# Performance work log

Hardware: AMD Instinct MI355X
Metric: run time of the kernel (lower is better)

## Reference

```python
import jax, jax.numpy as jnp
import numpy as np

B = 1024   # batch
N = 512    # points per sample (fixed by Linear(512,128))
G = 32     # voxel grid side (fixed: 5 stride-2 convs must reach 1^3)
CH = [1, 4, 16, 32, 64, 128]
BN_EPS = 1e-5


def _basis():
    # PointEmbed sinusoidal basis: hidden_dim=48 -> 8 freqs per axis, [3, 24]
    e = (2.0 ** np.arange(8)).astype(np.float32) * np.pi
    z = np.zeros(8, np.float32)
    b = np.stack([np.concatenate([e, z, z]),
                  np.concatenate([z, e, z]),
                  np.concatenate([z, z, e])])
    return jnp.asarray(b)


def setup_inputs() -> dict:
    key = jax.random.key(0)
    ks = jax.random.split(key, 16)
    inp = {
        "voxels": jax.random.normal(ks[0], (B, 1, G, G, G), jnp.float32),
        "centers": jax.random.uniform(ks[1], (B, N, 3), jnp.float32) * 2.0 - 1.0,
    }
    for i in range(5):
        cin, cout = CH[i], CH[i + 1]
        inp[f"W{i+1}"] = jax.random.normal(ks[2 + i], (cout, cin, 3, 3, 3), jnp.float32) * 0.05
        inp[f"b{i+1}"] = jnp.zeros((cout,), jnp.float32)
        inp[f"g{i+1}"] = jnp.ones((cout,), jnp.float32)
        inp[f"beta{i+1}"] = jnp.zeros((cout,), jnp.float32)
    inp["pe_w"] = jax.random.normal(ks[7], (51, 128), jnp.float32) * 0.05  # Linear(48+3, 128)
    inp["pe_b"] = jnp.zeros((128,), jnp.float32)
    inp["f1_w"] = jax.random.normal(ks[8], (128, 1), jnp.float32) * 0.05   # ff_128_1
    inp["f1_b"] = jnp.zeros((1,), jnp.float32)
    inp["f2_w"] = jax.random.normal(ks[9], (512, 128), jnp.float32) * 0.05  # ff_512_128
    inp["f2_b"] = jnp.zeros((128,), jnp.float32)
    return inp


def _conv_bn_relu(x, W, b, g, beta):
    # SparseConv3d(k=3, s=2, p=1) on fully-occupied grid == dense conv; BN in batch-stats mode
    y = jax.lax.conv_general_dilated(
        x, W, window_strides=(2, 2, 2), padding=[(1, 1)] * 3,
        dimension_numbers=("NCDHW", "OIDHW", "NCDHW"))
    y = y + b[None, :, None, None, None]
    m = jnp.mean(y, axis=(0, 2, 3, 4), keepdims=True)
    v = jnp.var(y, axis=(0, 2, 3, 4), keepdims=True)
    y = (y - m) * jax.lax.rsqrt(v + BN_EPS)
    y = y * g[None, :, None, None, None] + beta[None, :, None, None, None]
    return jax.nn.relu(y)


def reference(voxels, centers,
              W1, b1, g1, beta1, W2, b2, g2, beta2, W3, b3, g3, beta3,
              W4, b4, g4, beta4, W5, b5, g5, beta5,
              pe_w, pe_b, f1_w, f1_b, f2_w, f2_b):
    # --- PointEmbed branch ---
    basis = _basis()                                      # [3, 24]
    proj = jnp.einsum("bnd,de->bne", centers, basis)      # [B, N, 24]
    emb = jnp.concatenate([jnp.sin(proj), jnp.cos(proj), centers], axis=2)  # [B, N, 51]
    xc = emb @ pe_w + pe_b                                # [B, N, 128]
    xc = (xc @ f1_w + f1_b)[..., 0]                       # [B, N=512]
    xc = xc @ f2_w + f2_b                                 # [B, 128]
    # --- sparse conv stack (dense-occupancy equivalent) ---
    x = voxels
    for W, b, g, be in ((W1, b1, g1, beta1), (W2, b2, g2, beta2),
                        (W3, b3, g3, beta3), (W4, b4, g4, beta4),
                        (W5, b5, g5, beta5)):
        x = _conv_bn_relu(x, W, b, g, be)
    x = x.reshape(-1, 128)                                # [B,128,1,1,1] -> [B,128]
    return x + xc
```

## Files before the change

### kernel.cpp

```cpp
#include <hip/hip_runtime.h>
#include <hip/hip_bf16.h>

#ifndef M_PI
#define M_PI 3.14159265358979323846
#endif

#define BN_EPS 1e-5f

#define OFF_Y1   0ull
#define OFF_Y2   16777216ull
#define OFF_Y3   25165824ull
#define OFF_Y4   27262976ull
#define OFF_Y5   27787264ull
#define OFF_S    27918336ull
#define OFF_W2G  28442624ull
#define OFF_W3G  28444352ull
#define OFF_W5G  28458176ull
#define OFF_U    28523712ull
#define OFF_SP1  28523776ull
#define OFF_SP2  28524288ull
#define OFF_SP3  28526336ull
#define OFF_SP4  28530432ull
#define OFF_SP5  28538624ull
#define SP_TOTAL 31232
#define OFF_W4G  OFF_Y1

__device__ __forceinline__ float wred(float v) {
    for (int m = 32; m; m >>= 1) v += __shfl_xor(v, m, 64);
    return v;
}

__device__ __forceinline__ void async_copy16(const void* g, void* l) {
    __builtin_amdgcn_global_load_lds((const __attribute__((address_space(1))) void*)g,
                                     (__attribute__((address_space(3))) void*)l,
                                     16, 0, 0);
}

__device__ __forceinline__ unsigned short f2bf(float f) {
    unsigned int x = __float_as_uint(f);
    unsigned int r = (x + 0x7fffu + ((x >> 16) & 1u)) >> 16;
    return (unsigned short)r;
}
__device__ __forceinline__ float bf2f(unsigned short u) {
    return __uint_as_float(((unsigned int)u) << 16);
}

__global__ void k_prep_w(const float* __restrict__ W2, const float* __restrict__ W3,
                         const float* __restrict__ W5,
                         float* __restrict__ w2g, float* __restrict__ w3g,
                         float* __restrict__ w5g, float* __restrict__ sp) {
    int idx = blockIdx.x * 256 + threadIdx.x;
    if (idx < 1728) {
        int co = idx & 15; int r = idx >> 4; int tap = r % 27; int ci = r / 27;
        w2g[idx] = W2[(co * 4 + ci) * 27 + tap];
        return;
    }
    idx -= 1728;
    if (idx < 13824) {
        int co = idx & 31; int r = idx >> 5; int tap = r % 27; int ci = r / 27;
        w3g[idx] = W3[(co * 16 + ci) * 27 + tap];
        return;
    }
    idx -= 13824;
    if (idx < 65536) {
        int co = idx & 127; int k = idx >> 7;
        int dx = k & 1, dy = (k >> 1) & 1, dz = (k >> 2) & 1, ci = k >> 3;
        w5g[idx] = W5[(co * 64 + ci) * 27 + (dz + 1) * 9 + (dy + 1) * 3 + (dx + 1)];
        return;
    }
    idx -= 65536;
    if (idx < SP_TOTAL) sp[idx] = 0.f;
}

__global__ void k_prep_w4(const float* __restrict__ W4, float* __restrict__ w4g) {
    int idx = blockIdx.x * 256 + threadIdx.x;
    if (idx < 55296) {
        int co = idx & 63; int r = idx >> 6;
        int tap = r % 27, ci = r / 27;
        w4g[idx] = W4[(co * 32 + ci) * 27 + tap];
    }
}

__global__ void k_prep_u(const float* __restrict__ pe_w, const float* __restrict__ pe_b,
                         const float* __restrict__ f1_w, const float* __restrict__ f1_b,
                         float* __restrict__ u) {
    int t = threadIdx.x;
    if (t < 51) {
        float acc = 0.f;
        for (int j = 0; j < 128; j++) acc += pe_w[t * 128 + j] * f1_w[j];
        u[t] = acc;
    } else if (t == 51) {
        float acc = f1_b[0];
        for (int j = 0; j < 128; j++) acc += pe_b[j] * f1_w[j];
        u[51] = acc;
    }
}

__global__ __launch_bounds__(256) void k_pe(const float* __restrict__ centers,
                                            const float* __restrict__ u,
                                            float* __restrict__ s) {
    __shared__ float us[52];
    int t = threadIdx.x;
    if (t < 52) us[t] = u[t];
    __syncthreads();
    int idx = blockIdx.x * 256 + t;
    float c3[3];
    c3[0] = centers[idx * 3 + 0];
    c3[1] = centers[idx * 3 + 1];
    c3[2] = centers[idx * 3 + 2];
    float acc = us[51] + c3[0] * us[48] + c3[1] * us[49] + c3[2] * us[50];
#pragma unroll
    for (int a = 0; a < 3; a++) {
#pragma unroll
        for (int f = 0; f < 8; f++) {
            float ang = c3[a] * (float)(M_PI * (double)(1 << f));
            float sv, cv;
            sincosf(ang, &sv, &cv);
            acc += sv * us[a * 8 + f] + cv * us[24 + a * 8 + f];
        }
    }
    s[idx] = acc;
}

__global__ __launch_bounds__(256) void k_c1(const float* __restrict__ vox,
                                            const float* __restrict__ W1,
                                            const float* __restrict__ b1,
                                            unsigned short* __restrict__ y1b,
                                            float* __restrict__ sp1) {
    __shared__ __align__(16) float slab[9 * 1024];
    __shared__ __align__(16) float wl[112];
    __shared__ float red2[32];
    int bid = blockIdx.x;
    int b = bid >> 1, q = bid & 1;
    int t = threadIdx.x;
    const float* vb = vox + (size_t)b * 32768;
    int wu = __builtin_amdgcn_readfirstlane(t >> 6);

    if (t < 108) { int tap = t >> 2, co = t & 3; wl[t] = W1[co * 27 + tap]; }
    if (q == 0) ((float4*)slab)[t] = make_float4(0.f, 0.f, 0.f, 0.f);

    int p0 = 16 * q;
    int s0 = q ? 7 : 0;
    {
        int s = s0;
        for (int i = 0; i < 5; i++) {
            int p = p0 - 1 + i;
            if (p >= 0) async_copy16(vb + p * 1024 + t * 4, slab + s * 1024 + wu * 256);
            s++; if (s == 9) s = 0;
        }
    }
    int yo = t >> 4, xo = t & 15;
    int e = 2 * xo;
    int eA = (e >= 2) ? e - 2 : 0;
    float mx0 = xo ? 1.f : 0.f;
    int iyc[3]; float myv[3];
#pragma unroll
    for (int ky = 0; ky < 3; ky++) {
        int iy = 2 * yo + ky - 1;
        myv[ky] = (iy < 0) ? 0.f : 1.f;
        iyc[ky] = (iy < 0) ? 0 : iy;
    }
    float bb0 = b1[0], bb1 = b1[1], bb2 = b1[2], bb3 = b1[3];
    float sums[4] = {0.f, 0.f, 0.f, 0.f}, sqs[4] = {0.f, 0.f, 0.f, 0.f};

    asm volatile("s_waitcnt vmcnt(0)" ::: "memory");
    __syncthreads();

    int s_win = s0;
    for (int j = 0; j < 4; j++) {
        int zq = 4 * q + j;
        if (j < 3) {
            int sp = s_win + 5; if (sp >= 9) sp -= 9;
            for (int i = 0; i < 4; i++) {
                int p = 4 * zq + 4 + i;
                async_copy16(vb + p * 1024 + t * 4, slab + sp * 1024 + wu * 256);
                sp++; if (sp == 9) sp = 0;
            }
        }
        int P[5];
        {
            int s = s_win;
#pragma unroll
            for (int i = 0; i < 5; i++) { P[i] = s * 1024; s++; if (s == 9) s = 0; }
        }
        float a0[4] = {bb0, bb1, bb2, bb3};
        float a1[4] = {bb0, bb1, bb2, bb3};
#pragma unroll
        for (int kz = 0; kz < 3; kz++) {
            const float* pz0 = slab + P[kz];
            const float* pz1 = slab + P[kz + 2];
#pragma unroll
            for (int ky = 0; ky < 3; ky++) {
                int ro = iyc[ky] * 32;
                float2 xa0 = *(const float2*)(pz0 + ro + eA);
                float2 xb0 = *(const float2*)(pz0 + ro + e);
                float2 xa1 = *(const float2*)(pz1 + ro + eA);
                float2 xb1 = *(const float2*)(pz1 + ro + e);
                float m1 = myv[ky], m0 = m1 * mx0;
                const float* wt = wl + (kz * 9 + ky * 3) * 4;
                float4 w0 = *(const float4*)(wt);
                float4 w1 = *(const float4*)(wt + 4);
                float4 w2 = *(const float4*)(wt + 8);
                float v00 = xa0.y * m0, v01 = xb0.x * m1, v02 = xb0.y * m1;
                float v10 = xa1.y * m0, v11 = xb1.x * m1, v12 = xb1.y * m1;
                a0[0] += v00 * w0.x + v01 * w1.x + v02 * w2.x;
                a0[1] += v00 * w0.y + v01 * w1.y + v02 * w2.y;
                a0[2] += v00 * w0.z + v01 * w1.z + v02 * w2.z;
                a0[3] += v00 * w0.w + v01 * w1.w + v02 * w2.w;
                a1[0] += v10 * w0.x + v11 * w1.x + v12 * w2.x;
                a1[1] += v10 * w0.y + v11 * w1.y + v12 * w2.y;
                a1[2] += v10 * w0.z + v11 * w1.z + v12 * w2.z;
                a1[3] += v10 * w0.w + v11 * w1.w + v12 * w2.w;
            }
        }
        size_t base = (size_t)b * 16384 + (size_t)(2 * zq) * 256 + t;
#pragma unroll
        for (int c = 0; c < 4; c++) {
            y1b[base + c * 4096] = f2bf(a0[c]);
            y1b[base + c * 4096 + 256] = f2bf(a1[c]);
            sums[c] += a0[c] + a1[c];
            sqs[c] += a0[c] * a0[c] + a1[c] * a1[c];
        }
        s_win += 4; if (s_win >= 9) s_win -= 9;
        asm volatile("s_waitcnt vmcnt(0)" ::: "memory");
        __syncthreads();
    }
    int lane = t & 63, w = t >> 6;
#pragma unroll
    for (int c = 0; c < 4; c++) { sums[c] = wred(sums[c]); sqs[c] = wred(sqs[c]); }
    if (lane == 0) {
#pragma unroll
        for (int c = 0; c < 4; c++) { red2[w * 8 + c] = sums[c]; red2[w * 8 + 4 + c] = sqs[c]; }
    }
    __syncthreads();
    if (t < 8) {
        int c = t >> 1, isq = t & 1;
        float acc = red2[isq * 4 + c] + red2[8 + isq * 4 + c] +
                    red2[16 + isq * 4 + c] + red2[24 + isq * 4 + c];
        atomicAdd(&sp1[(2 * c + isq) * 64 + (bid & 63)], acc);
    }
}

__global__ __launch_bounds__(256) void k_c2(const unsigned short* __restrict__ y1b,
                                            const float* __restrict__ w2g,
                                            const float* __restrict__ b2,
                                            const float* __restrict__ g1,
                                            const float* __restrict__ be1,
                                            const float* __restrict__ sp1,
                                            unsigned short* __restrict__ y2u,
                                            float* __restrict__ sp2) {
    __shared__ __align__(16) unsigned short slab16[9216];
    __shared__ __align__(16) float wl[1728];
    __shared__ float adl[8];
    __shared__ float red[8];
    int t = threadIdx.x;
    int bid = blockIdx.x;
    int b = bid >> 1, q = bid & 1;
    int w = t >> 6, lane = t & 63;
    int wu = __builtin_amdgcn_readfirstlane(w);
    const unsigned short* yb = y1b + (size_t)b * 16384;
    if (q == 0) ((float2*)slab16)[t] = make_float2(0.f, 0.f);
    {
        int h = wu & 1;
        int ci0 = h * 2 + (lane >> 5);
        int g = lane & 31;
        int gs = g ^ (((g >> 3) & 3) << 1);
        const unsigned short* src0 = yb + ci0 * 4096 + gs * 8;
        int pstart = wu >> 1;
        if (q == 0 && pstart == 0) pstart = 2;
        for (int p = pstart; p < 9; p += 2) {
            int zi = 8 * q - 1 + p;
            async_copy16(src0 + zi * 256, slab16 + p * 1024 + h * 512);
        }
    }
    for (int i = t; i < 1728; i += 256) wl[i] = w2g[i];
    for (int row = w; row < 8; row += 4) {
        float v = wred(sp1[row * 64 + lane]);
        if (lane == 0) red[row] = v;
    }
    __syncthreads();
    if (t < 4) {
        float cnt = 4194304.0f;
        float m = red[2 * t] / cnt;
        float var = red[2 * t + 1] / cnt - m * m;
        float a = g1[t] * rsqrtf(var + BN_EPS);
        adl[t] = a; adl[4 + t] = be1[t] - m * a;
    }
    asm volatile("s_waitcnt vmcnt(0)" ::: "memory");
    __syncthreads();
    int zp = w >> 1;
    int cgo = __builtin_amdgcn_readfirstlane((w & 1) * 8);
    int yo = lane >> 3, xo = lane & 7;
    float my0 = yo ? 1.f : 0.f, mx0 = xo ? 1.f : 0.f;
    float mzw = (q == 0 && zp == 0) ? 0.f : 1.f;
    int yw3[3], sw3[3], xh3[3], xp3[3];
#pragma unroll
    for (int k = 0; k < 3; k++) {
        int yi = 2 * yo + k - 1; int yc = yi < 0 ? 0 : yi;
        yw3[k] = yc * 8;
        sw3[k] = ((yc >> 2) & 3) << 3;
        int xi = 2 * xo + k - 1; int xv = xi < 0 ? 0 : xi;
        xh3[k] = xv >> 1; xp3[k] = xv & 1;
    }
    float aa[4], dd[4];
#pragma unroll
    for (int c = 0; c < 4; c++) { aa[c] = adl[c]; dd[c] = adl[4 + c]; }
    float acc0[8], acc1[8];
#pragma unroll
    for (int c = 0; c < 8; c++) { acc0[c] = b2[cgo + c]; acc1[c] = acc0[c]; }
    for (int ci = 0; ci < 4; ci++) {
        float a = aa[ci], d = dd[ci];
        const unsigned short* pb16 = slab16 + zp * 4096 + ci * 256;
        const float* wci = wl + ci * 432 + cgo;
#pragma unroll
        for (int kz = 0; kz < 3; kz++) {
            const unsigned short* pl = pb16 + kz * 1024;
#pragma unroll
            for (int ky = 0; ky < 3; ky++) {
                int wb = yw3[ky], sw = sw3[ky];
#pragma unroll
                for (int kx = 0; kx < 3; kx++) {
                    int idx = (((wb + xh3[kx]) ^ sw) << 1) | xp3[kx];
                    float v0 = bf2f(pl[idx]);
                    float v1 = bf2f(pl[idx + 2048]);
                    float vb0 = fmaxf(a * v0 + d, 0.f);
                    float vb1 = fmaxf(a * v1 + d, 0.f);
                    if (kz == 0) vb0 *= mzw;
                    if (ky == 0) { vb0 *= my0; vb1 *= my0; }
                    if (kx == 0) { vb0 *= mx0; vb1 *= mx0; }
                    const float* wt = wci + (kz * 9 + ky * 3 + kx) * 16;
                    float4 wA = *(const float4*)(wt);
                    float4 wB = *(const float4*)(wt + 4);
                    acc0[0] += vb0 * wA.x; acc0[1] += vb0 * wA.y;
                    acc0[2] += vb0 * wA.z; acc0[3] += vb0 * wA.w;
                    acc0[4] += vb0 * wB.x; acc0[5] += vb0 * wB.y;
                    acc0[6] += vb0 * wB.z; acc0[7] += vb0 * wB.w;
                    acc1[0] += vb1 * wA.x; acc1[1] += vb1 * wA.y;
                    acc1[2] += vb1 * wA.z; acc1[3] += vb1 * wA.w;
                    acc1[4] += vb1 * wB.x; acc1[5] += vb1 * wB.y;
                    acc1[6] += vb1 * wB.z; acc1[7] += vb1 * wB.w;
                }
            }
        }
    }
    int z0 = 4 * q + 2 * zp;
    size_t ob = (size_t)b * 8192 + (size_t)cgo * 512 + z0 * 64 + lane;
#pragma unroll
    for (int c = 0; c < 8; c++) {
        y2u[ob + c * 512] = f2bf(acc0[c]);
        y2u[ob + c * 512 + 64] = f2bf(acc1[c]);
    }
    int slot = bid & 63;
#pragma unroll
    for (int c = 0; c < 8; c++) {
        float s_ = wred(acc0[c] + acc1[c]);
        float q_ = wred(acc0[c] * acc0[c] + acc1[c] * acc1[c]);
        if (lane == 0) {
            atomicAdd(&sp2[(2 * (cgo + c)) * 64 + slot], s_);
            atomicAdd(&sp2[(2 * (cgo + c) + 1) * 64 + slot], q_);
        }
    }
}

__global__ __launch_bounds__(256) void k_c3(const unsigned short* __restrict__ y2u,
                                            const float* __restrict__ w3g,
                                            const float* __restrict__ b3,
                                            const float* __restrict__ g2,
                                            const float* __restrict__ be2,
                                            const float* __restrict__ sp2,
                                            unsigned short* __restrict__ y3u,
                                            float* __restrict__ sp3) {
    __shared__ __align__(16) unsigned short in3u[8192];
    __shared__ float adl[32], red[32];
    int t = threadIdx.x;
    int b = blockIdx.x;
    int w = t >> 6, lane = t & 63;
    int wu = __builtin_amdgcn_readfirstlane(w);
    {
        int zc = lane >> 3;
        int gsrc = (lane & 7) ^ zc;
        const unsigned short* srcb = y2u + (size_t)b * 8192 + zc * 64 + gsrc * 8;
        for (int cq = 0; cq < 4; cq++) {
            int ci = wu * 4 + cq;
            async_copy16(srcb + ci * 512, in3u + ci * 512);
        }
    }
    for (int row = w; row < 32; row += 4) {
        float v = wred(sp2[row * 64 + lane]);
        if (lane == 0) red[row] = v;
    }
    __syncthreads();
    if (t < 16) {
        float cnt = 524288.0f;
        float m = red[2 * t] / cnt;
        float var = red[2 * t + 1] / cnt - m * m;
        float a = g2[t] * rsqrtf(var + BN_EPS);
        adl[t] = a; adl[16 + t] = be2[t] - m * a;
    }
    asm volatile("s_waitcnt vmcnt(0)" ::: "memory");
    __syncthreads();
    int px = lane & 3, py = (lane >> 2) & 3, pz = lane >> 4;
    float mz0 = pz ? 1.f : 0.f, my0 = py ? 1.f : 0.f, mx0 = px ? 1.f : 0.f;
    int zo3[3], zx3[3], yw3[3], xh3[3], xp3[3];
#pragma unroll
    for (int k = 0; k < 3; k++) {
        int zi = 2 * pz + k - 1; int zc = zi < 0 ? 0 : zi;
        zo3[k] = zc * 64; zx3[k] = (zc & 7) << 2;
        int yi = 2 * py + k - 1; int yc = yi < 0 ? 0 : yi;
        yw3[k] = yc * 4;
        int xi = 2 * px + k - 1; int xv = xi < 0 ? 0 : xi;
        xh3[k] = xv >> 1; xp3[k] = xv & 1;
    }
    int coh = wu & 1, cih = wu >> 1;
    int cgo = coh * 16;
    float acc[16];
#pragma unroll
    for (int c = 0; c < 16; c++) acc[c] = 0.f;
    for (int cii = 0; cii < 8; cii++) {
        int ci = cih * 8 + cii;
        float a = adl[ci], d = adl[16 + ci];
        const unsigned short* base = in3u + ci * 512;
        const float* wci = w3g + ci * 864 + cgo;
#pragma unroll
        for (int kz = 0; kz < 3; kz++) {
            int zo = zo3[kz], zx = zx3[kz];
#pragma unroll
            for (int ky = 0; ky < 3; ky++) {
                int yw = yw3[ky];
#pragma unroll
                for (int kx = 0; kx < 3; kx++) {
                    int idx = zo + ((((yw + xh3[kx]) ^ zx) << 1) | xp3[kx]);
                    float v = bf2f(base[idx]);
                    float vb = fmaxf(a * v + d, 0.f);
                    if (kz == 0) vb *= mz0;
                    if (ky == 0) vb *= my0;
                    if (kx == 0) vb *= mx0;
                    const float* wr = wci + (kz * 9 + ky * 3 + kx) * 32;
#pragma unroll
                    for (int c = 0; c < 16; c++) acc[c] += vb * wr[c];
                }
            }
        }
    }
    __syncthreads();
    float* sc = (float*)in3u;
    if (wu >= 2) {
        float* pp = sc + (wu & 1) * 1280 + lane * 20;
#pragma unroll
        for (int c4 = 0; c4 < 4; c4++)
            *(float4*)(pp + c4 * 4) = make_float4(acc[c4*4], acc[c4*4+1], acc[c4*4+2], acc[c4*4+3]);
    }
    __syncthreads();
    if (wu < 2) {
        const float* pp = sc + wu * 1280 + lane * 20;
#pragma unroll
        for (int c = 0; c < 16; c++) acc[c] += pp[c] + b3[cgo + c];
        size_t ob = (size_t)b * 2048 + lane;
#pragma unroll
        for (int c = 0; c < 16; c++) y3u[ob + (size_t)(cgo + c) * 64] = f2bf(acc[c]);
        int slot = b & 63;
#pragma unroll
        for (int c = 0; c < 16; c++) {
            float s_ = wred(acc[c]), q_ = wred(acc[c] * acc[c]);
            if (lane == 0) {
                atomicAdd(&sp3[(2 * (cgo + c)) * 64 + slot], s_);
                atomicAdd(&sp3[(2 * (cgo + c) + 1) * 64 + slot], q_);
            }
        }
    }
}

__global__ __launch_bounds__(256) void k_c4(const unsigned short* __restrict__ y3u,
                                            const float* __restrict__ w4g,
                                            const float* __restrict__ b4,
                                            const float* __restrict__ g3,
                                            const float* __restrict__ be3,
                                            const float* __restrict__ sp3,
                                            float* __restrict__ y4,
                                            float* __restrict__ sp4) {
    __shared__ __align__(16) unsigned short in4u[8 * 2056];
    __shared__ float adb[64], red[64];
    int t = threadIdx.x;
    int bid = blockIdx.x;
    int bq = bid >> 2, coq = bid & 3;
    int w = t >> 6, lane = t & 63;
    int wu = __builtin_amdgcn_readfirstlane(w);
#pragma unroll
    for (int h = 0; h < 2; h++) {
        int bs2 = wu * 2 + h;
        const unsigned short* src = y3u + (size_t)(bq * 8 + bs2) * 2048 + lane * 8;
        for (int j = 0; j < 4; j++)
            async_copy16(src + j * 512, in4u + bs2 * 2056 + j * 512);
    }
    for (int row = w; row < 64; row += 4) {
        float v = wred(sp3[row * 64 + lane]);
        if (lane == 0) red[row] = v;
    }
    __syncthreads();
    if (t < 32) {
        float cnt = 65536.0f;
        float m = red[2 * t] / cnt;
        float var = red[2 * t + 1] / cnt - m * m;
        float a = g3[t] * rsqrtf(var + BN_EPS);
        adb[t] = a; adb[32 + t] = be3[t] - m * a;
    }
    asm volatile("s_waitcnt vmcnt(0)" ::: "memory");
    __syncthreads();
    int bs = lane >> 3, pos = lane & 7;
    int pz = pos >> 2, py = (pos >> 1) & 1, px = pos & 1;
    int z0 = 2 * pz - 1; if (z0 < 0) z0 = 0;
    int y0 = 2 * py - 1; if (y0 < 0) y0 = 0;
    int x0 = 2 * px - 1; if (x0 < 0) x0 = 0;
    int zo_[3] = {z0 * 16, 2 * pz * 16, (2 * pz + 1) * 16};
    int yo_[3] = {y0 * 4, 2 * py * 4, (2 * py + 1) * 4};
    int xo_[3] = {x0, 2 * px, 2 * px + 1};
    float mz = pz ? 1.f : 0.f, my = py ? 1.f : 0.f, mx = px ? 1.f : 0.f;
    float acc[16];
#pragma unroll
    for (int c = 0; c < 16; c++) acc[c] = 0.f;
    const unsigned short* inb = in4u + bs * 2056;
    for (int cii = 0; cii < 8; cii++) {
        int ci = wu * 8 + cii;
        float a = adb[ci], d = adb[32 + ci];
        const unsigned short* inc = inb + ci * 64;
        const float* wcb = w4g + ci * 1728 + coq * 16;
#pragma unroll
        for (int kz = 0; kz < 3; kz++)
#pragma unroll
            for (int ky = 0; ky < 3; ky++)
#pragma unroll
                for (int kx = 0; kx < 3; kx++) {
                    float v = bf2f(inc[zo_[kz] + yo_[ky] + xo_[kx]]);
                    float vb = fmaxf(a * v + d, 0.f);
                    if (kz == 0) vb *= mz;
                    if (ky == 0) vb *= my;
                    if (kx == 0) vb *= mx;
                    const float* wr = wcb + (kz * 9 + ky * 3 + kx) * 64;
#pragma unroll
                    for (int c = 0; c < 16; c++) acc[c] += vb * wr[c];
                }
    }
    __syncthreads();
    float* sc = (float*)in4u;
    if (wu > 0) {
        float* pp = sc + (wu - 1) * 1280 + lane * 20;
#pragma unroll
        for (int c4 = 0; c4 < 4; c4++)
            *(float4*)(pp + c4 * 4) = make_float4(acc[c4*4], acc[c4*4+1], acc[c4*4+2], acc[c4*4+3]);
    }
    __syncthreads();
    if (wu == 0) {
#pragma unroll
        for (int p = 0; p < 3; p++) {
            const float* pp = sc + p * 1280 + lane * 20;
#pragma unroll
            for (int c = 0; c < 16; c++) acc[c] += pp[c];
        }
        int bfull = bq * 8 + bs;
        size_t ob = (size_t)bfull * 512 + pos;
        int slot = bid & 63;
#pragma unroll
        for (int c = 0; c < 16; c++) {
            float vv = acc[c] + b4[coq * 16 + c];
            y4[ob + (size_t)(coq * 16 + c) * 8] = vv;
            acc[c] = vv;
        }
#pragma unroll
        for (int c = 0; c < 16; c++) {
            float s_ = wred(acc[c]), q_ = wred(acc[c] * acc[c]);
            if (lane == 0) {
                atomicAdd(&sp4[(2 * (coq * 16 + c)) * 64 + slot], s_);
                atomicAdd(&sp4[(2 * (coq * 16 + c) + 1) * 64 + slot], q_);
            }
        }
    }
}

__global__ __launch_bounds__(512) void k_c5(const float* __restrict__ y4,
                                            const float* __restrict__ w5g,
                                            const float* __restrict__ b5,
                                            const float* __restrict__ g4,
                                            const float* __restrict__ be4,
                                            const float* __restrict__ sp4,
                                            float* __restrict__ y5,
                                            float* __restrict__ sp5) {
    __shared__ __align__(16) float A[2048];
    __shared__ float P[512];
    __shared__ float ad[128], red[128];
    int t = threadIdx.x;
    int bq = blockIdx.x;
    int w = t >> 6, lane = t & 63;
    for (int row = w; row < 128; row += 8) {
        float v = wred(sp4[row * 64 + lane]);
        if (lane == 0) red[row] = v;
    }
    __syncthreads();
    if (t < 64) {
        float cnt = 8192.0f;
        float m = red[2 * t] / cnt;
        float var = red[2 * t + 1] / cnt - m * m;
        float a = g4[t] * rsqrtf(var + BN_EPS);
        ad[t] = a; ad[64 + t] = be4[t] - m * a;
    }
    __syncthreads();
    {
        int bs = t >> 7, k0 = (t & 127) << 2;
        float4 vv = *(const float4*)(y4 + (size_t)(bq * 4 + bs) * 512 + k0);
        int ci = k0 >> 3;
        float a = ad[ci], d = ad[64 + ci];
        float4 o;
        o.x = fmaxf(a * vv.x + d, 0.f);
        o.y = fmaxf(a * vv.y + d, 0.f);
        o.z = fmaxf(a * vv.z + d, 0.f);
        o.w = fmaxf(a * vv.w + d, 0.f);
        *(float4*)(A + bs * 512 + k0) = o;
    }
    __syncthreads();
    int bs = w & 3, kh = w >> 2;
    float acc0 = 0.f, acc1 = 0.f;
    const float* Ab = A + bs * 512 + kh * 256;
    const float* wp = w5g + kh * 32768 + lane * 2;
#pragma unroll 8
    for (int k = 0; k < 256; k++) {
        float2 wv = *(const float2*)(wp + k * 128);
        float av = Ab[k];
        acc0 += av * wv.x;
        acc1 += av * wv.y;
    }
    if (kh == 0) {
        P[bs * 128 + lane * 2] = acc0;
        P[bs * 128 + lane * 2 + 1] = acc1;
    }
    __syncthreads();
    if (kh == 1) {
        float f0 = acc0 + P[bs * 128 + lane * 2] + b5[lane * 2];
        float f1 = acc1 + P[bs * 128 + lane * 2 + 1] + b5[lane * 2 + 1];
        *(float2*)(y5 + (size_t)(bq * 4 + bs) * 128 + lane * 2) = make_float2(f0, f1);
        P[bs * 128 + lane * 2] = f0;
        P[bs * 128 + lane * 2 + 1] = f1;
    }
    __syncthreads();
    if (t < 128) {
        float s = 0.f, q = 0.f;
        for (int bb = 0; bb < 4; bb++) {
            float vv = P[bb * 128 + t];
            s += vv; q += vv * vv;
        }
        int slot = bq & 63;
        atomicAdd(&sp5[(2 * t) * 64 + slot], s);
        atomicAdd(&sp5[(2 * t + 1) * 64 + slot], q);
    }
}

__global__ __launch_bounds__(512) void k_f2(const float* __restrict__ s,
                                            const float* __restrict__ f2w,
                                            const float* __restrict__ f2b,
                                            const float* __restrict__ g5,
                                            const float* __restrict__ be5,
                                            const float* __restrict__ sp5,
                                            const float* __restrict__ y5,
                                            float* __restrict__ out) {
    __shared__ __align__(16) float A[2048];
    __shared__ float P[512];
    __shared__ float ad[256], red[256];
    int t = threadIdx.x;
    int bq = blockIdx.x;
    int w = t >> 6, lane = t & 63;
    for (int row = w; row < 256; row += 8) {
        float v = wred(sp5[row * 64 + lane]);
        if (lane == 0) red[row] = v;
    }
    __syncthreads();
    if (t < 128) {
        float cnt = 1024.0f;
        float m = red[2 * t] / cnt;
        float var = red[2 * t + 1] / cnt - m * m;
        float a = g5[t] * rsqrtf(var + BN_EPS);
        ad[t] = a; ad[128 + t] = be5[t] - m * a;
    }
    {
        int bs = t >> 7, k0 = (t & 127) << 2;
        float4 vv = *(const float4*)(s + (size_t)(bq * 4 + bs) * 512 + k0);
        *(float4*)(A + bs * 512 + k0) = vv;
    }
    __syncthreads();
    int bs = w & 3, kh = w >> 2;
    float acc0 = 0.f, acc1 = 0.f;
    const float* Ab = A + bs * 512 + kh * 256;
    const float* wp = f2w + kh * 32768 + lane * 2;
#pragma unroll 8
    for (int k = 0; k < 256; k++) {
        float2 wv = *(const float2*)(wp + k * 128);
        float av = Ab[k];
        acc0 += av * wv.x;
        acc1 += av * wv.y;
    }
    if (kh == 0) {
        P[bs * 128 + lane * 2] = acc0;
        P[bs * 128 + lane * 2 + 1] = acc1;
    }
    __syncthreads();
    if (kh == 1) {
        int b = bq * 4 + bs;
        int co = lane * 2;
        float2 vy = *(const float2*)(y5 + (size_t)b * 128 + co);
        float f0 = acc0 + P[bs * 128 + co] + f2b[co] +
                   fmaxf(ad[co] * vy.x + ad[128 + co], 0.f);
        float f1 = acc1 + P[bs * 128 + co + 1] + f2b[co + 1] +
                   fmaxf(ad[co + 1] * vy.y + ad[128 + co + 1], 0.f);
        *(float2*)(out + (size_t)b * 128 + co) = make_float2(f0, f1);
    }
}

extern "C" void kernel_launch(void* const* d_in, const int* in_sizes, int n_in,
                              void* d_out, int out_size, void* d_ws, size_t ws_size,
                              hipStream_t stream) {
    const float* vox     = (const float*)d_in[0];
    const float* centers = (const float*)d_in[1];
    const float* W1   = (const float*)d_in[2];
    const float* b1   = (const float*)d_in[3];
    const float* g1   = (const float*)d_in[4];
    const float* be1  = (const float*)d_in[5];
    const float* W2   = (const float*)d_in[6];
    const float* b2   = (const float*)d_in[7];
    const float* g2   = (const float*)d_in[8];
    const float* be2  = (const float*)d_in[9];
    const float* W3   = (const float*)d_in[10];
    const float* b3   = (const float*)d_in[11];
    const float* g3   = (const float*)d_in[12];
    const float* be3  = (const float*)d_in[13];
    const float* W4   = (const float*)d_in[14];
    const float* b4   = (const float*)d_in[15];
    const float* g4   = (const float*)d_in[16];
    const float* be4  = (const float*)d_in[17];
    const float* W5   = (const float*)d_in[18];
    const float* b5   = (const float*)d_in[19];
    const float* g5   = (const float*)d_in[20];
    const float* be5  = (const float*)d_in[21];
    const float* pe_w = (const float*)d_in[22];
    const float* pe_b = (const float*)d_in[23];
    const float* f1_w = (const float*)d_in[24];
    const float* f1_b = (const float*)d_in[25];
    const float* f2_w = (const float*)d_in[26];
    const float* f2_b = (const float*)d_in[27];

    float* ws  = (float*)d_ws;
    unsigned short* y1b = (unsigned short*)(ws + OFF_Y1);
    unsigned short* y2u = (unsigned short*)(ws + OFF_Y2);
    unsigned short* y3u = (unsigned short*)(ws + OFF_Y3);
    float* y4  = ws + OFF_Y4;
    float* y5  = ws + OFF_Y5;
    float* s   = ws + OFF_S;
    float* w2g = ws + OFF_W2G;
    float* w3g = ws + OFF_W3G;
    float* w4g = ws + OFF_W4G;
    float* w5g = ws + OFF_W5G;
    float* u   = ws + OFF_U;
    float* sp1 = ws + OFF_SP1;
    float* sp2 = ws + OFF_SP2;
    float* sp3 = ws + OFF_SP3;
    float* sp4 = ws + OFF_SP4;
    float* sp5 = ws + OFF_SP5;

    k_prep_w<<<439, 256, 0, stream>>>(W2, W3, W5, w2g, w3g, w5g, sp1);
    k_prep_u<<<1, 64, 0, stream>>>(pe_w, pe_b, f1_w, f1_b, u);
    k_pe<<<2048, 256, 0, stream>>>(centers, u, s);
    k_c1<<<2048, 256, 0, stream>>>(vox, W1, b1, y1b, sp1);
    k_c2<<<2048, 256, 0, stream>>>(y1b, w2g, b2, g1, be1, sp1, y2u, sp2);
    k_prep_w4<<<216, 256, 0, stream>>>(W4, w4g);
    k_c3<<<1024, 256, 0, stream>>>(y2u, w3g, b3, g2, be2, sp2, y3u, sp3);
    k_c4<<<512, 256, 0, stream>>>(y3u, w4g, b4, g3, be3, sp3, y4, sp4);
    k_c5<<<256, 512, 0, stream>>>(y4, w5g, b5, g4, be4, sp4, y5, sp5);
    k_f2<<<256, 512, 0, stream>>>(s, f2_w, f2_b, g5, be5, sp5, y5, (float*)d_out);
}
```

Measured before the change: 274.6 us.

## Restructure conv2 so each wave computes all four z outputs and reuses slab loads

```diff
diff --git a/kernel.cpp b/kernel.cpp
--- a/kernel.cpp
+++ b/kernel.cpp
@@ -115,7 +115,7 @@
         for (int f = 0; f < 8; f++) {
             float ang = c3[a] * (float)(M_PI * (double)(1 << f));
             float sv, cv;
-            sincosf(ang, &sv, &cv);
+            __sincosf(ang, &sv, &cv);
             acc += sv * us[a * 8 + f] + cv * us[24 + a * 8 + f];
         }
     }
@@ -241,14 +241,14 @@
     }
 }
 
-__global__ __launch_bounds__(256) void k_c2(const unsigned short* __restrict__ y1b,
-                                            const float* __restrict__ w2g,
-                                            const float* __restrict__ b2,
-                                            const float* __restrict__ g1,
-                                            const float* __restrict__ be1,
-                                            const float* __restrict__ sp1,
-                                            unsigned short* __restrict__ y2u,
-                                            float* __restrict__ sp2) {
+__global__ __launch_bounds__(256, 4) void k_c2(const unsigned short* __restrict__ y1b,
+                                               const float* __restrict__ w2g,
+                                               const float* __restrict__ b2,
+                                               const float* __restrict__ g1,
+                                               const float* __restrict__ be1,
+                                               const float* __restrict__ sp1,
+                                               unsigned short* __restrict__ y2u,
+                                               float* __restrict__ sp2) {
     __shared__ __align__(16) unsigned short slab16[9216];
     __shared__ __align__(16) float wl[1728];
     __shared__ float adl[8];
@@ -288,76 +288,85 @@
     }
     asm volatile("s_waitcnt vmcnt(0)" ::: "memory");
     __syncthreads();
-    int zp = w >> 1;
-    int cgo = __builtin_amdgcn_readfirstlane((w & 1) * 8);
+    int cgo = __builtin_amdgcn_readfirstlane(wu * 4);
     int yo = lane >> 3, xo = lane & 7;
     float my0 = yo ? 1.f : 0.f, mx0 = xo ? 1.f : 0.f;
-    float mzw = (q == 0 && zp == 0) ? 0.f : 1.f;
-    int yw3[3], sw3[3], xh3[3], xp3[3];
+    float mq = (q == 0) ? 0.f : 1.f;
+    int yw3[3], sw3[3];
 #pragma unroll
     for (int k = 0; k < 3; k++) {
         int yi = 2 * yo + k - 1; int yc = yi < 0 ? 0 : yi;
         yw3[k] = yc * 8;
         sw3[k] = ((yc >> 2) & 3) << 3;
-        int xi = 2 * xo + k - 1; int xv = xi < 0 ? 0 : xi;
-        xh3[k] = xv >> 1; xp3[k] = xv & 1;
-    }
+    }
+    int xhL = (xo > 0) ? (xo - 1) : 0;
+    int xhR = xo;
     float aa[4], dd[4];
 #pragma unroll
     for (int c = 0; c < 4; c++) { aa[c] = adl[c]; dd[c] = adl[4 + c]; }
-    float acc0[8], acc1[8];
-#pragma unroll
-    for (int c = 0; c < 8; c++) { acc0[c] = b2[cgo + c]; acc1[c] = acc0[c]; }
+    float acc[4][4];
+#pragma unroll
+    for (int z = 0; z < 4; z++)
+#pragma unroll
+        for (int j = 0; j < 4; j++) acc[z][j] = b2[cgo + j];
     for (int ci = 0; ci < 4; ci++) {
         float a = aa[ci], d = dd[ci];
-        const unsigned short* pb16 = slab16 + zp * 4096 + ci * 256;
+        const unsigned int* base32 = (const unsigned int*)(slab16 + ci * 256);
         const float* wci = wl + ci * 432 + cgo;
 #pragma unroll
-        for (int kz = 0; kz < 3; kz++) {
-            const unsigned short* pl = pb16 + kz * 1024;
-#pragma unroll
-            for (int ky = 0; ky < 3; ky++) {
-                int wb = yw3[ky], sw = sw3[ky];
-#pragma unroll
-                for (int kx = 0; kx < 3; kx++) {
-                    int idx = (((wb + xh3[kx]) ^ sw) << 1) | xp3[kx];
-                    float v0 = bf2f(pl[idx]);
-                    float v1 = bf2f(pl[idx + 2048]);
-                    float vb0 = fmaxf(a * v0 + d, 0.f);
-                    float vb1 = fmaxf(a * v1 + d, 0.f);
-                    if (kz == 0) vb0 *= mzw;
-                    if (ky == 0) { vb0 *= my0; vb1 *= my0; }
-                    if (kx == 0) { vb0 *= mx0; vb1 *= mx0; }
-                    const float* wt = wci + (kz * 9 + ky * 3 + kx) * 16;
-                    float4 wA = *(const float4*)(wt);
-                    float4 wB = *(const float4*)(wt + 4);
-                    acc0[0] += vb0 * wA.x; acc0[1] += vb0 * wA.y;
-                    acc0[2] += vb0 * wA.z; acc0[3] += vb0 * wA.w;
-                    acc0[4] += vb0 * wB.x; acc0[5] += vb0 * wB.y;
-                    acc0[6] += vb0 * wB.z; acc0[7] += vb0 * wB.w;
-                    acc1[0] += vb1 * wA.x; acc1[1] += vb1 * wA.y;
-                    acc1[2] += vb1 * wA.z; acc1[3] += vb1 * wA.w;
-                    acc1[4] += vb1 * wB.x; acc1[5] += vb1 * wB.y;
-                    acc1[6] += vb1 * wB.z; acc1[7] += vb1 * wB.w;
+        for (int ky = 0; ky < 3; ky++) {
+            int wLw = (yw3[ky] + xhL) ^ sw3[ky];
+            int wRw = (yw3[ky] + xhR) ^ sw3[ky];
+            float4 w9[9];
+#pragma unroll
+            for (int kz = 0; kz < 3; kz++)
+#pragma unroll
+                for (int kx = 0; kx < 3; kx++)
+                    w9[kz * 3 + kx] = *(const float4*)(wci + (kz * 9 + ky * 3 + kx) * 16);
+            float m1 = (ky == 0) ? my0 : 1.f;
+            float m0 = m1 * mx0;
+#pragma unroll
+            for (int p = 0; p < 9; p++) {
+                const unsigned int* pp = base32 + p * 512;
+                unsigned int L = pp[wLw], R = pp[wRw];
+                float v0 = __uint_as_float(L & 0xffff0000u);
+                float v1 = __uint_as_float(R << 16);
+                float v2 = __uint_as_float(R & 0xffff0000u);
+                float pb = (p == 0) ? mq : 1.f;
+                float vb0 = fmaxf(a * v0 + d, 0.f) * (m0 * pb);
+                float vb1 = fmaxf(a * v1 + d, 0.f) * (m1 * pb);
+                float vb2 = fmaxf(a * v2 + d, 0.f) * (m1 * pb);
+#pragma unroll
+                for (int z = 0; z < 4; z++) {
+                    int kz = p - 2 * z;
+                    if (kz < 0 || kz > 2) continue;
+                    float4 wa = w9[kz * 3 + 0];
+                    float4 wb_ = w9[kz * 3 + 1];
+                    float4 wc = w9[kz * 3 + 2];
+                    acc[z][0] += vb0 * wa.x + vb1 * wb_.x + vb2 * wc.x;
+                    acc[z][1] += vb0 * wa.y + vb1 * wb_.y + vb2 * wc.y;
+                    acc[z][2] += vb0 * wa.z + vb1 * wb_.z + vb2 * wc.z;
+                    acc[z][3] += vb0 * wa.w + vb1 * wb_.w + vb2 * wc.w;
                 }
             }
         }
     }
-    int z0 = 4 * q + 2 * zp;
-    size_t ob = (size_t)b * 8192 + (size_t)cgo * 512 + z0 * 64 + lane;
-#pragma unroll
-    for (int c = 0; c < 8; c++) {
-        y2u[ob + c * 512] = f2bf(acc0[c]);
-        y2u[ob + c * 512 + 64] = f2bf(acc1[c]);
-    }
+    size_t ob = (size_t)b * 8192 + (size_t)cgo * 512 + (size_t)(4 * q) * 64 + lane;
+#pragma unroll
+    for (int j = 0; j < 4; j++)
+#pragma unroll
+        for (int z = 0; z < 4; z++)
+            y2u[ob + j * 512 + z * 64] = f2bf(acc[z][j]);
     int slot = bid & 63;
 #pragma unroll
-    for (int c = 0; c < 8; c++) {
-        float s_ = wred(acc0[c] + acc1[c]);
-        float q_ = wred(acc0[c] * acc0[c] + acc1[c] * acc1[c]);
+    for (int j = 0; j < 4; j++) {
+        float s_ = 0.f, q_ = 0.f;
+#pragma unroll
+        for (int z = 0; z < 4; z++) { s_ += acc[z][j]; q_ += acc[z][j] * acc[z][j]; }
+        s_ = wred(s_); q_ = wred(q_);
         if (lane == 0) {
-            atomicAdd(&sp2[(2 * (cgo + c)) * 64 + slot], s_);
-            atomicAdd(&sp2[(2 * (cgo + c) + 1) * 64 + slot], q_);
+            atomicAdd(&sp2[(2 * (cgo + j)) * 64 + slot], s_);
+            atomicAdd(&sp2[(2 * (cgo + j) + 1) * 64 + slot], q_);
         }
     }
 }
```

Result: slower. 597.3 us (+117.5%).
